# Kernel optimization log

Measured on AMD Instinct MI355X. Metric: run time of the kernel, lower is better.

Reference implementation:

```python
import jax, jax.numpy as jnp
import numpy as np

EMB_DIM = 256
ATT_DIM = 256
B, S = 8, 2048


def setup_inputs() -> dict:
    key = jax.random.key(0)
    ks = jax.random.split(key, 9)
    scale = 1.0 / np.sqrt(EMB_DIM)
    inp = {
        "x": jax.random.normal(ks[0], (B, S, EMB_DIM), dtype=jnp.float32),
        "mask": jax.random.randint(ks[1], (B, S, S), 0, 2, dtype=jnp.int32),
        "Wq": jax.random.uniform(ks[2], (EMB_DIM, ATT_DIM), jnp.float32, -scale, scale),
        "bq": jax.random.uniform(ks[3], (ATT_DIM,), jnp.float32, -scale, scale),
        "Wk": jax.random.uniform(ks[4], (EMB_DIM, ATT_DIM), jnp.float32, -scale, scale),
        "bk": jax.random.uniform(ks[5], (ATT_DIM,), jnp.float32, -scale, scale),
        "Wv": jax.random.uniform(ks[6], (EMB_DIM, ATT_DIM), jnp.float32, -scale, scale),
        "bv": jax.random.uniform(ks[7], (ATT_DIM,), jnp.float32, -scale, scale),
    }
    return inp


def reference(x, mask, Wq, bq, Wk, bk, Wv, bv):
    # Linear projections: (B,S,E) @ (E,A) + (A,)
    q = jnp.einsum("bse,ea->bsa", x, Wq) + bq
    k = jnp.einsum("bse,ea->bsa", x, Wk) + bk
    v = jnp.einsum("bse,ea->bsa", x, Wv) + bv
    # scores: (B,S,S)
    scores = jnp.einsum("bqa,bka->bqk", q, k) / jnp.sqrt(jnp.float32(ATT_DIM))
    scores = jnp.where(mask == 0, jnp.float32(-1e9), scores)
    attn = jax.nn.softmax(scores, axis=-1)
    return jnp.einsum("bqk,bka->bqa", attn, v)
```

## Files before the change

kernel.cpp:

```cpp
#include <hip/hip_runtime.h>
#include <hip/hip_bf16.h>
#include <stdint.h>

#define BATCH 8
#define SEQ   2048
#define EMB   256
#define ADIM  256

typedef __bf16 bf16_t;
typedef __attribute__((ext_vector_type(8))) __bf16 bf16x8;
typedef __attribute__((ext_vector_type(4))) float  f32x4;
typedef uint32_t u32;

static __device__ __forceinline__ f32x4 mfma16(bf16x8 a, bf16x8 b, f32x4 c) {
    return __builtin_amdgcn_mfma_f32_16x16x32_bf16(a, b, c, 0, 0, 0);
}

static __device__ __forceinline__ void gld16(const void* g, void* l) {
    __builtin_amdgcn_global_load_lds((const __attribute__((address_space(1))) u32*)g,
                                     (__attribute__((address_space(3))) u32*)l, 16, 0, 0);
}

__global__ __launch_bounds__(256) void wtkv_kernel(const float* __restrict__ Wk,
                                                   const float* __restrict__ Wv,
                                                   bf16_t* __restrict__ wt) {
    int tid = blockIdx.x * 256 + threadIdx.x;
    int m = tid >> 16;
    int i = tid & 65535;
    int a = i >> 8, e = i & 255;
    const float* W = (m == 0) ? Wk : Wv;
    wt[m * 65536 + a * 256 + e] = (bf16_t)W[e * 256 + a];
}

__global__ __launch_bounds__(128, 2) void proj_kv(const float* __restrict__ x,
                                                  const bf16_t* __restrict__ wt,
                                                  const float* __restrict__ bk,
                                                  const float* __restrict__ bv,
                                                  char* __restrict__ Ksw,
                                                  char* __restrict__ Vsw) {
    const int tid  = threadIdx.x;
    const int wid  = tid >> 6;
    const int lane = tid & 63;
    const int lq   = lane >> 4;
    const int ln   = lane & 15;
    const int wp   = blockIdx.x & 1;
    const int mbase = (blockIdx.x >> 1) * 32 + wid * 16;
    const bf16_t* w    = wt + wp * 65536;
    const float*  bias = wp ? bv : bk;

    bf16x8 xf[8];
    const float* xp = x + (size_t)(mbase + ln) * EMB;
    #pragma unroll
    for (int c = 0; c < 8; ++c) {
        f32x4 a = *(const f32x4*)(xp + c * 32 + lq * 8);
        f32x4 b = *(const f32x4*)(xp + c * 32 + lq * 8 + 4);
        bf16x8 v;
        v[0] = (bf16_t)a[0]; v[1] = (bf16_t)a[1]; v[2] = (bf16_t)a[2]; v[3] = (bf16_t)a[3];
        v[4] = (bf16_t)b[0]; v[5] = (bf16_t)b[1]; v[6] = (bf16_t)b[2]; v[7] = (bf16_t)b[3];
        xf[c] = v;
    }

    f32x4 acc[16];
    #pragma unroll
    for (int t = 0; t < 16; ++t) acc[t] = (f32x4){0.f, 0.f, 0.f, 0.f};

    #pragma unroll
    for (int c = 0; c < 8; ++c) {
        #pragma unroll
        for (int t = 0; t < 16; ++t) {
            bf16x8 wf = *(const bf16x8*)(w + (size_t)(t * 16 + ln) * 256 + c * 32 + lq * 8);
            acc[t] = mfma16(xf[c], wf, acc[t]);
        }
    }

    if (wp == 0) {
        #pragma unroll
        for (int t = 0; t < 16; ++t) {
            float bb = bias[t * 16 + ln];
            int cb = t * 2 + (ln >> 3);
            int j  = ln & 7;
            #pragma unroll
            for (int r = 0; r < 4; ++r) {
                int s = mbase + lq * 4 + r;
                int b = s >> 11, sb = s & 2047;
                int tile = sb >> 5, n = sb & 31;
                *(bf16_t*)(Ksw + (size_t)b * 1048576 + (size_t)tile * 16384 + n * 512 +
                           (((cb ^ (n & 7))) * 16) + j * 2) = (bf16_t)(acc[t][r] + bb);
            }
        }
    } else {
        const int vswz_l = (ln & 3) ^ ((ln >> 2) & 3);
        #pragma unroll
        for (int t = 0; t < 16; ++t) {
            float bb = bias[t * 16 + ln];
            int a = t * 16 + ln;
            #pragma unroll
            for (int r = 0; r < 4; ++r) {
                int s = mbase + lq * 4 + r;
                int b = s >> 11, sb = s & 2047;
                int tile = sb >> 5, k = sb & 31;
                int lqv = k >> 3, j = k & 7;
                *(bf16_t*)(Vsw + (size_t)b * 1048576 + (size_t)tile * 16384 + a * 64 +
                           ((lqv ^ vswz_l) * 16) + j * 2) = (bf16_t)(acc[t][r] + bb);
            }
        }
    }
}

__global__ __launch_bounds__(256, 2) void flash_kernel(const float* __restrict__ x,
                                                       const float* __restrict__ WqM,
                                                       const float* __restrict__ bq,
                                                       const char* __restrict__ Ksw,
                                                       const char* __restrict__ Vsw,
                                                       int* __restrict__ mask,
                                                       float* __restrict__ out) {
    __shared__ __align__(16) char smem[71168];
    const int tid  = threadIdx.x;
    const int wid  = tid >> 6;
    const int lane = tid & 63;
    const int lq   = lane >> 4;
    const int ln   = lane & 15;
    const int qw   = wid >> 1;
    const int kw   = wid & 1;
    const int batch = blockIdx.x & 7;
    const int kvh   = (blockIdx.x >> 3) & 1;
    const int qbase = (blockIdx.x >> 4) * 64;

    const char* Kb = Ksw + (size_t)batch * 1048576 + (size_t)(kvh * 32) * 16384;
    const char* Vb = Vsw + (size_t)batch * 1048576 + (size_t)(kvh * 32) * 16384;
    char*  Pq_ = smem + 65536 + qw * 2560;
    char*  Pt  = smem + 65536 + wid * 1280;
    float* Ls  = (float*)(smem + 70656);

    const char* kg0 = Kb + wid * 4096 + lane * 16;
    const char* vg0 = Vb + wid * 4096 + lane * 16;

    int* mroot = mask + (size_t)batch * SEQ * SEQ +
                 (size_t)(qbase + qw * 32) * SEQ + kvh * 1024 + kw * 16 + ln;

    {
        char* kl = smem + wid * 4096;
        char* vl = smem + 16384 + wid * 4096;
        #pragma unroll
        for (int i = 0; i < 4; ++i) gld16(kg0 + i * 1024, kl + i * 1024);
        #pragma unroll
        for (int i = 0; i < 4; ++i) gld16(vg0 + i * 1024, vl + i * 1024);
    }
    int mv[2][2][4];
    #pragma unroll
    for (int w = 0; w < 2; ++w)
        #pragma unroll
        for (int h = 0; h < 2; ++h)
            #pragma unroll
            for (int r = 0; r < 4; ++r)
                mv[w][h][r] = mroot[(size_t)(h * 16 + lq * 4 + r) * SEQ + w * 32];

    bf16x8 qf[2][8];
    {
        bf16x8 xf[2][8];
        #pragma unroll
        for (int h = 0; h < 2; ++h) {
            const float* xp = x + (size_t)(batch * SEQ + qbase + qw * 32 + h * 16 + ln) * EMB;
            #pragma unroll
            for (int c = 0; c < 8; ++c) {
                f32x4 a = *(const f32x4*)(xp + c * 32 + lq * 8);
                f32x4 b = *(const f32x4*)(xp + c * 32 + lq * 8 + 4);
                bf16x8 v;
                v[0] = (bf16_t)a[0]; v[1] = (bf16_t)a[1]; v[2] = (bf16_t)a[2]; v[3] = (bf16_t)a[3];
                v[4] = (bf16_t)b[0]; v[5] = (bf16_t)b[1]; v[6] = (bf16_t)b[2]; v[7] = (bf16_t)b[3];
                xf[h][c] = v;
            }
        }
        f32x4 qacc[2][16];
        #pragma unroll
        for (int h = 0; h < 2; ++h)
            #pragma unroll
            for (int t = 0; t < 16; ++t) qacc[h][t] = (f32x4){0.f, 0.f, 0.f, 0.f};

        char* Wsp = smem + 32768;
        const int e = ln & 7;
        #pragma unroll 1
        for (int cp = 0; cp < 8; ++cp) {
            __syncthreads();
            const float* wqp = WqM + (size_t)(cp * 32) * 256 + tid;
            #pragma unroll
            for (int i = 0; i < 4; ++i) {
                bf16x8 pk;
                #pragma unroll
                for (int j = 0; j < 8; ++j)
                    pk[j] = (bf16_t)wqp[(size_t)(i * 8 + j) * 256];
                *(bf16x8*)(Wsp + tid * 128 + ((i ^ (tid & 7)) * 16)) = pk;
            }
            __syncthreads();
            #pragma unroll
            for (int t = 0; t < 16; ++t) {
                bf16x8 wf = *(const bf16x8*)(Wsp + (t * 16 + ln) * 128 + ((lq ^ e) * 16));
                qacc[0][t] = mfma16(xf[0][cp], wf, qacc[0][t]);
                qacc[1][t] = mfma16(xf[1][cp], wf, qacc[1][t]);
            }
        }
        #pragma unroll
        for (int h = 0; h < 2; ++h) {
            #pragma unroll
            for (int c = 0; c < 8; ++c) {
                #pragma unroll
                for (int half2 = 0; half2 < 2; ++half2) {
                    int t = 2 * c + half2;
                    float bb = bq[t * 16 + ln];
                    #pragma unroll
                    for (int r = 0; r < 4; ++r) {
                        float v = (qacc[h][t][r] + bb) * 0.0625f;
                        ((bf16_t*)(Pt + (lq * 4 + r) * 80))[half2 * 16 + ln] = (bf16_t)v;
                    }
                }
                qf[h][c] = *(const bf16x8*)(Pt + ln * 80 + lq * 16);
            }
        }
    }

    f32x4 o[2][8];
    #pragma unroll
    for (int h = 0; h < 2; ++h)
        #pragma unroll
        for (int t = 0; t < 8; ++t) o[h][t] = (f32x4){0.f, 0.f, 0.f, 0.f};
    float lsum[2][4] = {{0.f,0.f,0.f,0.f},{0.f,0.f,0.f,0.f}};

    const int kswz = ln & 7;
    const int vswz = (lq ^ (ln & 3) ^ ((ln >> 2) & 3)) * 16;
    const int n0   = kw * 16 + ln;

    for (int kt = 0; kt < 32; ++kt) {
        __syncthreads();
        if (kt + 1 < 32) {
            int nb = (kt + 1) & 1;
            const char* kg = kg0 + (size_t)(kt + 1) * 16384;
            const char* vg = vg0 + (size_t)(kt + 1) * 16384;
            char* kl = smem + nb * 32768 + wid * 4096;
            char* vl = smem + nb * 32768 + 16384 + wid * 4096;
            #pragma unroll
            for (int i = 0; i < 4; ++i) gld16(kg + i * 1024, kl + i * 1024);
            #pragma unroll
            for (int i = 0; i < 4; ++i) gld16(vg + i * 1024, vl + i * 1024);
        }
        const int buf = kt & 1;
        const char* Ksb = smem + buf * 32768;
        const char* Vsb = smem + buf * 32768 + 16384;

        f32x4 s0 = (f32x4){0.f,0.f,0.f,0.f};
        f32x4 s1 = (f32x4){0.f,0.f,0.f,0.f};
        const char* krow = Ksb + n0 * 512;
        #pragma unroll
        for (int c = 0; c < 8; ++c) {
            bf16x8 kf = *(const bf16x8*)(krow + (((c * 4 + lq) ^ kswz) * 16));
            s0 = mfma16(qf[0][c], kf, s0);
            s1 = mfma16(qf[1][c], kf, s1);
        }

        const int (*mc)[4] = mv[kt & 1];
        #pragma unroll
        for (int r = 0; r < 4; ++r) {
            float p0 = mc[0][r] ? __expf(s0[r]) : 0.f;
            float p1 = mc[1][r] ? __expf(s1[r]) : 0.f;
            lsum[0][r] += p0;
            lsum[1][r] += p1;
            ((bf16_t*)(Pq_ + (lq * 4 + r) * 80))[kw * 16 + ln]      = (bf16_t)p0;
            ((bf16_t*)(Pq_ + (16 + lq * 4 + r) * 80))[kw * 16 + ln] = (bf16_t)p1;
        }

        {
            const int ktn = (kt + 2 < 32) ? kt + 2 : 31;
            int (*md)[4] = mv[kt & 1];
            #pragma unroll
            for (int h = 0; h < 2; ++h)
                #pragma unroll
                for (int r = 0; r < 4; ++r)
                    md[h][r] = mroot[(size_t)(h * 16 + lq * 4 + r) * SEQ + ktn * 32];
        }

        asm volatile("s_waitcnt lgkmcnt(0)\n\ts_barrier" ::: "memory");

        bf16x8 pa0 = *(const bf16x8*)(Pq_ + ln * 80 + lq * 16);
        bf16x8 pa1 = *(const bf16x8*)(Pq_ + (16 + ln) * 80 + lq * 16);

        const char* vbase = Vsb + (kw * 128 + ln) * 64 + vswz;
        #pragma unroll
        for (int t = 0; t < 8; ++t) {
            bf16x8 vf = *(const bf16x8*)(vbase + t * 1024);
            o[0][t] = mfma16(pa0, vf, o[0][t]);
            o[1][t] = mfma16(pa1, vf, o[1][t]);
        }
    }

    __syncthreads();
    #pragma unroll
    for (int h = 0; h < 2; ++h) {
        #pragma unroll
        for (int r = 0; r < 4; ++r) {
            float v = lsum[h][r];
            v += __shfl_xor(v, 1);
            v += __shfl_xor(v, 2);
            v += __shfl_xor(v, 4);
            v += __shfl_xor(v, 8);
            if (ln == 0) Ls[(qw * 2 + kw) * 32 + h * 16 + lq * 4 + r] = v;
            lsum[h][r] = v;
        }
    }
    __syncthreads();

    if (kw == 0 && ln == 0) {
        #pragma unroll
        for (int h = 0; h < 2; ++h)
            #pragma unroll
            for (int r = 0; r < 4; ++r) {
                int row = h * 16 + lq * 4 + r;
                float tot = lsum[h][r] + Ls[(qw * 2 + 1) * 32 + row];
                ((float*)mask)[(size_t)batch * SEQ * SEQ +
                               (size_t)(qbase + qw * 32 + row) * SEQ + kvh * 1024] = tot;
            }
    }

    #pragma unroll
    for (int h = 0; h < 2; ++h) {
        #pragma unroll
        for (int r = 0; r < 4; ++r) {
            float* orow = out + (size_t)(batch * SEQ + qbase + qw * 32 + h * 16 + lq * 4 + r) * ADIM
                          + kw * 128 + ln;
            #pragma unroll
            for (int t = 0; t < 8; ++t)
                atomicAdd(orow + t * 16, o[h][t][r]);
        }
    }
}

__global__ __launch_bounds__(256) void merge_kernel(const float* __restrict__ lbuf,
                                                    float* __restrict__ out) {
    int idx  = blockIdx.x * 256 + threadIdx.x;
    int base = idx * 4;
    int row  = base >> 8;
    int b = row >> 11, r = row & 2047;
    float l0 = lbuf[(size_t)b * SEQ * SEQ + (size_t)r * SEQ];
    float l1 = lbuf[(size_t)b * SEQ * SEQ + (size_t)r * SEQ + 1024];
    float inv = 1.0f / (l0 + l1);
    f32x4 v = *(const f32x4*)(out + base);
    v[0] *= inv; v[1] *= inv; v[2] *= inv; v[3] *= inv;
    *(f32x4*)(out + base) = v;
}

extern "C" void kernel_launch(void* const* d_in, const int* in_sizes, int n_in,
                              void* d_out, int out_size, void* d_ws, size_t ws_size,
                              hipStream_t stream) {
    const float* x    = (const float*)d_in[0];
    int*         mask = (int*)d_in[1];
    const float* Wq   = (const float*)d_in[2];
    const float* bq   = (const float*)d_in[3];
    const float* Wk   = (const float*)d_in[4];
    const float* bk   = (const float*)d_in[5];
    const float* Wv   = (const float*)d_in[6];
    const float* bv   = (const float*)d_in[7];
    float* out = (float*)d_out;

    char* Ksw = (char*)d_ws;
    char* Vsw = Ksw + (size_t)8 * 1024 * 1024;
    bf16_t* wt = (bf16_t*)d_out;

    wtkv_kernel<<<512, 256, 0, stream>>>(Wk, Wv, wt);
    proj_kv<<<1024, 128, 0, stream>>>(x, wt, bk, bv, Ksw, Vsw);
    hipMemsetAsync(d_out, 0, (size_t)out_size * sizeof(float), stream);
    flash_kernel<<<512, 256, 0, stream>>>(x, Wq, bq, Ksw, Vsw, mask, out);
    merge_kernel<<<4096, 256, 0, stream>>>((const float*)mask, out);
}
```

Measured before the change: 380.1 us.

## Compute K and V in one block and stage outputs through LDS for vector stores

Each proj_kv block now computes both the K and V projections for its 32 rows, so the x fragments are loaded and converted to bf16 once instead of twice, and the grid is halved. Results are staged per wave in shared memory and then written to the swizzled global K/V layouts as 16-byte vector stores, replacing scattered 2-byte stores. Occupancy hint drops to 1 block per CU and the kernel gains 20KB of LDS. Only lgkmcnt waits are used, with no barrier, which relies on each wave reading back only its own staging region.

```diff
diff --git a/kernel.cpp b/kernel.cpp
--- a/kernel.cpp
+++ b/kernel.cpp
@@ -32,77 +32,102 @@
     wt[m * 65536 + a * 256 + e] = (bf16_t)W[e * 256 + a];
 }
 
-__global__ __launch_bounds__(128, 2) void proj_kv(const float* __restrict__ x,
+__global__ __launch_bounds__(128, 1) void proj_kv(const float* __restrict__ x,
                                                   const bf16_t* __restrict__ wt,
                                                   const float* __restrict__ bk,
                                                   const float* __restrict__ bv,
                                                   char* __restrict__ Ksw,
                                                   char* __restrict__ Vsw) {
+    __shared__ __align__(16) char stg[2][10240];
     const int tid  = threadIdx.x;
     const int wid  = tid >> 6;
     const int lane = tid & 63;
     const int lq   = lane >> 4;
     const int ln   = lane & 15;
-    const int wp   = blockIdx.x & 1;
-    const int mbase = (blockIdx.x >> 1) * 32 + wid * 16;
-    const bf16_t* w    = wt + wp * 65536;
-    const float*  bias = wp ? bv : bk;
+    const int blk  = blockIdx.x;
+    const int b    = blk >> 6;
+    const int tile = blk & 63;
+    const int mbase = blk * 32 + wid * 16;
+    char* S = stg[wid];
 
     bf16x8 xf[8];
     const float* xp = x + (size_t)(mbase + ln) * EMB;
     #pragma unroll
     for (int c = 0; c < 8; ++c) {
-        f32x4 a = *(const f32x4*)(xp + c * 32 + lq * 8);
-        f32x4 b = *(const f32x4*)(xp + c * 32 + lq * 8 + 4);
+        f32x4 a0 = *(const f32x4*)(xp + c * 32 + lq * 8);
+        f32x4 a1 = *(const f32x4*)(xp + c * 32 + lq * 8 + 4);
         bf16x8 v;
-        v[0] = (bf16_t)a[0]; v[1] = (bf16_t)a[1]; v[2] = (bf16_t)a[2]; v[3] = (bf16_t)a[3];
-        v[4] = (bf16_t)b[0]; v[5] = (bf16_t)b[1]; v[6] = (bf16_t)b[2]; v[7] = (bf16_t)b[3];
+        v[0] = (bf16_t)a0[0]; v[1] = (bf16_t)a0[1]; v[2] = (bf16_t)a0[2]; v[3] = (bf16_t)a0[3];
+        v[4] = (bf16_t)a1[0]; v[5] = (bf16_t)a1[1]; v[6] = (bf16_t)a1[2]; v[7] = (bf16_t)a1[3];
         xf[c] = v;
     }
 
     f32x4 acc[16];
+
     #pragma unroll
     for (int t = 0; t < 16; ++t) acc[t] = (f32x4){0.f, 0.f, 0.f, 0.f};
-
-    #pragma unroll
-    for (int c = 0; c < 8; ++c) {
-        #pragma unroll
-        for (int t = 0; t < 16; ++t) {
-            bf16x8 wf = *(const bf16x8*)(w + (size_t)(t * 16 + ln) * 256 + c * 32 + lq * 8);
-            acc[t] = mfma16(xf[c], wf, acc[t]);
-        }
-    }
-
-    if (wp == 0) {
-        #pragma unroll
-        for (int t = 0; t < 16; ++t) {
-            float bb = bias[t * 16 + ln];
-            int cb = t * 2 + (ln >> 3);
-            int j  = ln & 7;
-            #pragma unroll
-            for (int r = 0; r < 4; ++r) {
-                int s = mbase + lq * 4 + r;
-                int b = s >> 11, sb = s & 2047;
-                int tile = sb >> 5, n = sb & 31;
-                *(bf16_t*)(Ksw + (size_t)b * 1048576 + (size_t)tile * 16384 + n * 512 +
-                           (((cb ^ (n & 7))) * 16) + j * 2) = (bf16_t)(acc[t][r] + bb);
-            }
-        }
-    } else {
-        const int vswz_l = (ln & 3) ^ ((ln >> 2) & 3);
-        #pragma unroll
-        for (int t = 0; t < 16; ++t) {
-            float bb = bias[t * 16 + ln];
-            int a = t * 16 + ln;
-            #pragma unroll
-            for (int r = 0; r < 4; ++r) {
-                int s = mbase + lq * 4 + r;
-                int b = s >> 11, sb = s & 2047;
-                int tile = sb >> 5, k = sb & 31;
-                int lqv = k >> 3, j = k & 7;
-                *(bf16_t*)(Vsw + (size_t)b * 1048576 + (size_t)tile * 16384 + a * 64 +
-                           ((lqv ^ vswz_l) * 16) + j * 2) = (bf16_t)(acc[t][r] + bb);
-            }
+    {
+        const bf16_t* w = wt;
+        #pragma unroll
+        for (int c = 0; c < 8; ++c)
+            #pragma unroll
+            for (int t = 0; t < 16; ++t) {
+                bf16x8 wf = *(const bf16x8*)(w + (size_t)(t * 16 + ln) * 256 + c * 32 + lq * 8);
+                acc[t] = mfma16(xf[c], wf, acc[t]);
+            }
+    }
+    #pragma unroll
+    for (int t = 0; t < 16; ++t) {
+        float bb = bk[t * 16 + ln];
+        #pragma unroll
+        for (int r = 0; r < 4; ++r)
+            *(bf16_t*)(S + (lq * 4 + r) * 512 + (t * 16 + ln) * 2) = (bf16_t)(acc[t][r] + bb);
+    }
+    asm volatile("s_waitcnt lgkmcnt(0)" ::: "memory");
+    {
+        char* Kg = Ksw + (size_t)b * 1048576 + (size_t)tile * 16384 + wid * 8192;
+        const int rh = lane >> 5;
+        const int p  = lane & 31;
+        #pragma unroll
+        for (int i = 0; i < 8; ++i) {
+            int row = i * 2 + rh;
+            int n   = wid * 16 + row;
+            int cb  = p ^ (n & 7);
+            f32x4 ch = *(const f32x4*)(S + row * 512 + cb * 16);
+            *(f32x4*)(Kg + row * 512 + p * 16) = ch;
+        }
+    }
+
+    #pragma unroll
+    for (int t = 0; t < 16; ++t) acc[t] = (f32x4){0.f, 0.f, 0.f, 0.f};
+    {
+        const bf16_t* w = wt + 65536;
+        #pragma unroll
+        for (int c = 0; c < 8; ++c)
+            #pragma unroll
+            for (int t = 0; t < 16; ++t) {
+                bf16x8 wf = *(const bf16x8*)(w + (size_t)(t * 16 + ln) * 256 + c * 32 + lq * 8);
+                acc[t] = mfma16(xf[c], wf, acc[t]);
+            }
+    }
+    #pragma unroll
+    for (int t = 0; t < 16; ++t) {
+        float bb = bv[t * 16 + ln];
+        #pragma unroll
+        for (int r = 0; r < 4; ++r)
+            *(bf16_t*)(S + (t * 16 + ln) * 40 + (lq * 4 + r) * 2) = (bf16_t)(acc[t][r] + bb);
+    }
+    asm volatile("s_waitcnt lgkmcnt(0)" ::: "memory");
+    {
+        char* Vg = Vsw + (size_t)b * 1048576 + (size_t)tile * 16384;
+        const int half = lane & 1;
+        const int kq   = wid * 2 + half;
+        #pragma unroll
+        for (int i = 0; i < 8; ++i) {
+            int a   = i * 32 + (lane >> 1);
+            int pos = kq ^ (a & 3) ^ ((a >> 2) & 3);
+            f32x4 ch = *(const f32x4*)(S + a * 40 + half * 16);
+            *(f32x4*)(Vg + a * 64 + pos * 16) = ch;
         }
     }
 }
@@ -364,7 +389,7 @@
     bf16_t* wt = (bf16_t*)d_out;
 
     wtkv_kernel<<<512, 256, 0, stream>>>(Wk, Wv, wt);
-    proj_kv<<<1024, 128, 0, stream>>>(x, wt, bk, bv, Ksw, Vsw);
+    proj_kv<<<512, 128, 0, stream>>>(x, wt, bk, bv, Ksw, Vsw);
     hipMemsetAsync(d_out, 0, (size_t)out_size * sizeof(float), stream);
     flash_kernel<<<512, 256, 0, stream>>>(x, Wq, bq, Ksw, Vsw, mask, out);
     merge_kernel<<<4096, 256, 0, stream>>>((const float*)mask, out);
```

Result: no change. 379.3 us (-0.2%).
